# Kernel tuning notes

Measured on AMD Instinct MI355X. Metric: run time of the kernel, lower is better.

## Reference

```python
import jax, jax.numpy as jnp
import numpy as np

N = 100_000      # nodes
E = 800_000      # edges (avg degree 8)
IN = 64          # in_channels
OUT = 64         # out_channels
HEADS = 4
HD = OUT // HEADS  # per-head out channels (concat=True)


def _unif(key, shape, fan_in):
    b = 1.0 / np.sqrt(fan_in)
    return jax.random.uniform(key, shape, jnp.float32, -b, b)


def setup_inputs() -> dict:
    key = jax.random.key(0)
    ks = jax.random.split(key, 12)
    x = jax.random.normal(ks[0], (N, IN), jnp.float32)
    pos = jax.random.normal(ks[1], (N, 3), jnp.float32)
    edge_index = jax.random.randint(ks[2], (2, E), 0, N, jnp.int32)
    # Per-head PointTransformerConv params (stacked over heads).
    # lin / lin_src / lin_dst are bias-free Linear(in, hd); pos_nn is Linear(3, hd) with bias.
    W_lin = _unif(ks[3], (HEADS, IN, HD), IN)
    W_src = _unif(ks[4], (HEADS, IN, HD), IN)
    W_dst = _unif(ks[5], (HEADS, IN, HD), IN)
    W_pos = _unif(ks[6], (HEADS, 3, HD), 3)
    b_pos = _unif(ks[7], (HEADS, HD), 3)
    # projection MLP: Linear(OUT,OUT) -> ReLU -> Linear(OUT,OUT)
    W1 = _unif(ks[8], (OUT, OUT), OUT)
    b1 = _unif(ks[9], (OUT,), OUT)
    W2 = _unif(ks[10], (OUT, OUT), OUT)
    b2 = _unif(ks[11], (OUT,), OUT)
    return dict(x=x, pos=pos, edge_index=edge_index, W_lin=W_lin, W_src=W_src,
                W_dst=W_dst, W_pos=W_pos, b_pos=b_pos, W1=W1, b1=b1, W2=W2, b2=b2)


def reference(x, pos, edge_index, W_lin, W_src, W_dst, W_pos, b_pos, W1, b1, W2, b2):
    # Add self-loops (PointTransformerConv default add_self_loops=True).
    loops = jnp.arange(N, dtype=edge_index.dtype)
    src = jnp.concatenate([edge_index[0], loops])   # j (source)
    dst = jnp.concatenate([edge_index[1], loops])   # i (target)

    # Per-node, all-heads projections: [N, H, HD]
    v = jnp.einsum('ni,hio->nho', x, W_lin)
    a_src = jnp.einsum('ni,hio->nho', x, W_src)
    a_dst = jnp.einsum('ni,hio->nho', x, W_dst)

    # Relative-position encoding delta = pos_nn(pos_i - pos_j): [Et, H, HD]
    rel = pos[dst] - pos[src]
    delta = jnp.einsum('ec,hco->eho', rel, W_pos) + b_pos

    # Attention logits per edge/channel: alpha_i - alpha_j + delta
    alpha = a_dst[dst] - a_src[src] + delta

    # Segment softmax over incoming edges of each target node (numerically stable).
    amax = jax.ops.segment_max(alpha, dst, num_segments=N)
    amax = jnp.where(jnp.isfinite(amax), amax, 0.0)
    ex = jnp.exp(alpha - amax[dst])
    denom = jax.ops.segment_sum(ex, dst, num_segments=N)
    attn = ex / jnp.maximum(denom[dst], 1e-16)

    # Message = attn * (lin(x_j) + delta), scatter-sum to targets: [N, H, HD]
    msg = attn * (v[src] + delta)
    out_h = jax.ops.segment_sum(msg, dst, num_segments=N)

    # Concat heads -> projection MLP
    out = out_h.reshape(N, HEADS * HD)
    h = jax.nn.relu(out @ W1 + b1)
    return h @ W2 + b2
```

## Files before the change

### kernel.cpp

```cpp
#include <hip/hip_runtime.h>
#include <math.h>


typedef _Float16 f16;
typedef _Float16 f16x2 __attribute__((ext_vector_type(2)));
typedef _Float16 f16x4 __attribute__((ext_vector_type(4)));
typedef _Float16 f16x8 __attribute__((ext_vector_type(8)));
typedef float f32x4 __attribute__((ext_vector_type(4)));

#define A_PITCH 104
#define LOG2E 1.44269504f
#define S_CAP 32

__global__ __launch_bounds__(256) void prep_hist_scatter_kernel(
    const int* __restrict__ ei, int E, int Hb,
    int* __restrict__ cnt, int* __restrict__ ssrc,
    const float* __restrict__ Ws, const float* __restrict__ Wl,
    const float* __restrict__ Wp, const float* __restrict__ bp,
    const float* __restrict__ W1, const float* __restrict__ W2,
    f16* __restrict__ Bt, f16* __restrict__ W1p, f16* __restrict__ W2p)
{
    if ((int)blockIdx.x < Hb) {
        int e = blockIdx.x * 256 + threadIdx.x;
        if (e < E) {
            int s = ei[e], d = ei[E + e];
            int r = atomicAdd(&cnt[d], 1);
            if (r < S_CAP) ssrc[d * S_CAP + r] = s;
        }
        return;
    }
    int idx = (blockIdx.x - Hb) * 256 + threadIdx.x;
    if (idx < 192 * 96) {
        int col = idx / 96, k = idx - col * 96;
        float v = 0.f;
        if (col < 128) {
            int p = col >> 1, h = p >> 4, o = p & 15;
            if (col & 1) {
                if (k < 64)      v = Wl[h * 1024 + k * 16 + o];
                else if (k < 67) v = -Wp[h * 48 + (k - 64) * 16 + o];
            } else {
                if (k < 64)      v = -LOG2E * Ws[h * 1024 + k * 16 + o];
                else if (k < 67) v = -LOG2E * Wp[h * 48 + (k - 64) * 16 + o];
            }
        } else {
            int c = col - 128, h = c >> 4, o = c & 15;
            if (k >= 64 && k < 67) v = Wp[h * 48 + (k - 64) * 16 + o];
            else if (k == 67)      v = bp[c];
        }
        Bt[col * 96 + k] = (f16)v;
    } else if (idx < 192 * 96 + 4096) {
        int t = idx - 192 * 96;
        int col = t >> 6, k = t & 63;
        W1p[col * 64 + k] = (f16)W1[k * 64 + col];
    } else if (idx < 192 * 96 + 8192) {
        int t = idx - 192 * 96 - 4096;
        int col = t >> 6, k = t & 63;
        W2p[col * 64 + k] = (f16)W2[k * 64 + col];
    }
}

__global__ __launch_bounds__(256) void gemm_kernel(
    const float* __restrict__ x, const float* __restrict__ pos,
    const f16* __restrict__ Bt, f16* __restrict__ P, int N)
{
    __shared__ f16 As[64 * A_PITCH];
    int tid = threadIdx.x;
    int l = tid & 63, wv = tid >> 6;
    int quad = l >> 4, lr = l & 15;
    int nb = blockIdx.x * 64;

    for (int it = 0; it < 4; it++) {
        int q = it * 256 + tid;
        int n = q >> 4, k = (q & 15) * 4;
        float4 xv = make_float4(0.f, 0.f, 0.f, 0.f);
        if (nb + n < N) xv = *(const float4*)&x[(size_t)(nb + n) * 64 + k];
        f16x4 h4; h4[0] = (f16)xv.x; h4[1] = (f16)xv.y; h4[2] = (f16)xv.z; h4[3] = (f16)xv.w;
        *(f16x4*)&As[n * A_PITCH + k] = h4;
    }
    {
        int n = tid >> 2, seg = tid & 3;
        f16x4 z = {(f16)0, (f16)0, (f16)0, (f16)0};
        f16x4 h4 = z;
        if (seg == 0 && nb + n < N) {
            h4[0] = (f16)pos[(size_t)(nb + n) * 3 + 0];
            h4[1] = (f16)pos[(size_t)(nb + n) * 3 + 1];
            h4[2] = (f16)pos[(size_t)(nb + n) * 3 + 2];
            h4[3] = (f16)1.0f;
        }
        *(f16x4*)&As[n * A_PITCH + 64 + seg * 8] = h4;
        *(f16x4*)&As[n * A_PITCH + 64 + seg * 8 + 4] = z;
    }
    __syncthreads();

    f16x8 af[4][3];
    #pragma unroll
    for (int mt = 0; mt < 4; mt++)
        #pragma unroll
        for (int kt = 0; kt < 3; kt++)
            af[mt][kt] = *(const f16x8*)&As[(mt * 16 + lr) * A_PITCH + kt * 32 + quad * 8];

    #pragma unroll
    for (int t = 0; t < 3; t++) {
        int colBase = (wv * 3 + t) * 16;
        f16x8 b0 = *(const f16x8*)&Bt[(colBase + lr) * 96 + 0  + quad * 8];
        f16x8 b1 = *(const f16x8*)&Bt[(colBase + lr) * 96 + 32 + quad * 8];
        f16x8 b2 = *(const f16x8*)&Bt[(colBase + lr) * 96 + 64 + quad * 8];
        #pragma unroll
        for (int mt = 0; mt < 4; mt++) {
            f32x4 acc = {0.f, 0.f, 0.f, 0.f};
            acc = __builtin_amdgcn_mfma_f32_16x16x32_f16(af[mt][0], b0, acc, 0, 0, 0);
            acc = __builtin_amdgcn_mfma_f32_16x16x32_f16(af[mt][1], b1, acc, 0, 0, 0);
            acc = __builtin_amdgcn_mfma_f32_16x16x32_f16(af[mt][2], b2, acc, 0, 0, 0);
            int col = colBase + lr;
            #pragma unroll
            for (int r = 0; r < 4; r++) {
                int row = nb + mt * 16 + quad * 4 + r;
                if (row < N) P[(size_t)row * 192 + col] = (f16)acc[r];
            }
        }
    }
}

__global__ __launch_bounds__(256) void attn_mlp_kernel(
    const f16* __restrict__ P,
    const int* __restrict__ cnt, const int* __restrict__ ssrc,
    const f16* __restrict__ W1p, const f16* __restrict__ W2p,
    const float* __restrict__ b1, const float* __restrict__ b2,
    float* __restrict__ out, int N)
{
    __shared__ f16 As[64 * 72];
    __shared__ f16 Hs[64 * 72];
    int tid = threadIdx.x, c = tid & 63, wv = tid >> 6;
    int quad = c >> 4, lr = c & 15;
    int nb = blockIdx.x * 64;

    const f16x2* AV = (const f16x2*)P;

    for (int t = 0; t < 16; t++) {
        int i = nb + wv * 16 + t;
        float oh = 0.f;
        if (i < N) {
            float Gi = (float)P[(size_t)i * 192 + 128 + c];
            f16x2 wi = AV[(size_t)i * 96 + c];
            float e0 = __builtin_amdgcn_exp2f((float)wi[0]);
            float num = e0 * (float)wi[1];
            float den = e0;
            int deg = cnt[i]; if (deg > S_CAP) deg = S_CAP;
            int base = i * S_CAP, k = 0;

#define EDGE_STEP(w)                                              \
            {                                                     \
                float e = __builtin_amdgcn_exp2f((float)w[0]);    \
                num = fmaf(e, (float)w[1], num);                  \
                den += e;                                         \
            }
            for (; k + 4 <= deg; k += 4) {
                int j0 = __builtin_amdgcn_readfirstlane(ssrc[base + k]);
                int j1 = __builtin_amdgcn_readfirstlane(ssrc[base + k + 1]);
                int j2 = __builtin_amdgcn_readfirstlane(ssrc[base + k + 2]);
                int j3 = __builtin_amdgcn_readfirstlane(ssrc[base + k + 3]);
                f16x2 w0 = AV[(size_t)j0 * 96 + c];
                f16x2 w1 = AV[(size_t)j1 * 96 + c];
                f16x2 w2 = AV[(size_t)j2 * 96 + c];
                f16x2 w3 = AV[(size_t)j3 * 96 + c];
                EDGE_STEP(w0); EDGE_STEP(w1); EDGE_STEP(w2); EDGE_STEP(w3);
            }
            for (; k < deg; k++) {
                int j = __builtin_amdgcn_readfirstlane(ssrc[base + k]);
                f16x2 w = AV[(size_t)j * 96 + c];
                EDGE_STEP(w);
            }
#undef EDGE_STEP
            oh = num / den + Gi;
        }
        As[(wv * 16 + t) * 72 + c] = (f16)oh;
    }
    __syncthreads();

    f16x8 af[4][2];
    #pragma unroll
    for (int mt = 0; mt < 4; mt++)
        #pragma unroll
        for (int kt = 0; kt < 2; kt++)
            af[mt][kt] = *(const f16x8*)&As[(mt * 16 + lr) * 72 + kt * 32 + quad * 8];

    int col = wv * 16 + lr;
    f16x8 wb0 = *(const f16x8*)&W1p[col * 64 + quad * 8];
    f16x8 wb1 = *(const f16x8*)&W1p[col * 64 + 32 + quad * 8];
    float bias1 = b1[col];
    #pragma unroll
    for (int mt = 0; mt < 4; mt++) {
        f32x4 acc = {0.f, 0.f, 0.f, 0.f};
        acc = __builtin_amdgcn_mfma_f32_16x16x32_f16(af[mt][0], wb0, acc, 0, 0, 0);
        acc = __builtin_amdgcn_mfma_f32_16x16x32_f16(af[mt][1], wb1, acc, 0, 0, 0);
        #pragma unroll
        for (int r = 0; r < 4; r++) {
            int row = mt * 16 + quad * 4 + r;
            Hs[row * 72 + col] = (f16)fmaxf(acc[r] + bias1, 0.f);
        }
    }
    __syncthreads();

    f16x8 ag[4][2];
    #pragma unroll
    for (int mt = 0; mt < 4; mt++)
        #pragma unroll
        for (int kt = 0; kt < 2; kt++)
            ag[mt][kt] = *(const f16x8*)&Hs[(mt * 16 + lr) * 72 + kt * 32 + quad * 8];

    f16x8 wc0 = *(const f16x8*)&W2p[col * 64 + quad * 8];
    f16x8 wc1 = *(const f16x8*)&W2p[col * 64 + 32 + quad * 8];
    float bias2 = b2[col];
    #pragma unroll
    for (int mt = 0; mt < 4; mt++) {
        f32x4 acc = {0.f, 0.f, 0.f, 0.f};
        acc = __builtin_amdgcn_mfma_f32_16x16x32_f16(ag[mt][0], wc0, acc, 0, 0, 0);
        acc = __builtin_amdgcn_mfma_f32_16x16x32_f16(ag[mt][1], wc1, acc, 0, 0, 0);
        #pragma unroll
        for (int r = 0; r < 4; r++) {
            int row = nb + mt * 16 + quad * 4 + r;
            if (row < N) out[(size_t)row * 64 + col] = acc[r] + bias2;
        }
    }
}

extern "C" void kernel_launch(void* const* d_in, const int* in_sizes, int n_in,
                              void* d_out, int out_size, void* d_ws, size_t ws_size,
                              hipStream_t stream)
{
    const float* x    = (const float*)d_in[0];
    const float* pos  = (const float*)d_in[1];
    const int*   ei   = (const int*)d_in[2];
    const float* Wl   = (const float*)d_in[3];
    const float* Ws   = (const float*)d_in[4];
    const float* Wp   = (const float*)d_in[6];
    const float* bpos = (const float*)d_in[7];
    const float* W1   = (const float*)d_in[8];
    const float* b1   = (const float*)d_in[9];
    const float* W2   = (const float*)d_in[10];
    const float* b2   = (const float*)d_in[11];
    float* out = (float*)d_out;

    const int N = in_sizes[0] / 64;
    const int E = in_sizes[2] / 2;

    char* w = (char*)d_ws;
    f16*  P    = (f16*)w;                   w += (size_t)N * 192 * 2;
    f16*  Bt   = (f16*)w;                   w += 192 * 96 * 2;
    f16*  W1p  = (f16*)w;                   w += 4096 * 2;
    f16*  W2p  = (f16*)w;                   w += 4096 * 2;
    int*  cnt  = (int*)w;                   w += (size_t)N * 4;
    int*  ssrc = (int*)w;

    const int Hb = (E + 255) / 256;
    const int Pb = (192 * 96 + 8192 + 255) / 256;

    hipMemsetAsync(cnt, 0, (size_t)N * sizeof(int), stream);

    prep_hist_scatter_kernel<<<Hb + Pb, 256, 0, stream>>>(
        ei, E, Hb, cnt, ssrc, Ws, Wl, Wp, bpos, W1, W2, Bt, W1p, W2p);
    gemm_kernel<<<(N + 63) / 64, 256, 0, stream>>>(x, pos, Bt, P, N);
    attn_mlp_kernel<<<(N + 63) / 64, 256, 0, stream>>>(P, cnt, ssrc, W1p, W2p,
                                                       b1, b2, out, N);
}
```

Measured before the change: 218.5 us.

## Split projection buffer into compact AV and G arrays, coalesce stores, shrink attention tiles

The GEMM output moves from one 192-wide buffer into a 128-wide AV array (gathered per edge) and a separate 64-wide G array. Results are staged through shared memory so global stores are coalesced 16-byte writes, and the edge gather now reads from a denser array. The attention kernel processes 32 nodes per block instead of 64, giving more blocks. Its edge loop becomes a single masked 4-wide loop, which is why the ssrc slots are now zeroed by an enlarged memset, adding extra memset traffic.

```diff
diff --git a/kernel.cpp b/kernel.cpp
--- a/kernel.cpp
+++ b/kernel.cpp
@@ -9,6 +9,7 @@
 typedef float f32x4 __attribute__((ext_vector_type(4)));
 
 #define A_PITCH 104
+#define C_PITCH 200
 #define LOG2E 1.44269504f
 #define S_CAP 32
 
@@ -61,9 +62,10 @@
 
 __global__ __launch_bounds__(256) void gemm_kernel(
     const float* __restrict__ x, const float* __restrict__ pos,
-    const f16* __restrict__ Bt, f16* __restrict__ P, int N)
-{
-    __shared__ f16 As[64 * A_PITCH];
+    const f16* __restrict__ Bt,
+    f16* __restrict__ AV, f16* __restrict__ G, int N)
+{
+    __shared__ f16 smem[64 * C_PITCH];
     int tid = threadIdx.x;
     int l = tid & 63, wv = tid >> 6;
     int quad = l >> 4, lr = l & 15;
@@ -75,7 +77,7 @@
         float4 xv = make_float4(0.f, 0.f, 0.f, 0.f);
         if (nb + n < N) xv = *(const float4*)&x[(size_t)(nb + n) * 64 + k];
         f16x4 h4; h4[0] = (f16)xv.x; h4[1] = (f16)xv.y; h4[2] = (f16)xv.z; h4[3] = (f16)xv.w;
-        *(f16x4*)&As[n * A_PITCH + k] = h4;
+        *(f16x4*)&smem[n * A_PITCH + k] = h4;
     }
     {
         int n = tid >> 2, seg = tid & 3;
@@ -87,8 +89,8 @@
             h4[2] = (f16)pos[(size_t)(nb + n) * 3 + 2];
             h4[3] = (f16)1.0f;
         }
-        *(f16x4*)&As[n * A_PITCH + 64 + seg * 8] = h4;
-        *(f16x4*)&As[n * A_PITCH + 64 + seg * 8 + 4] = z;
+        *(f16x4*)&smem[n * A_PITCH + 64 + seg * 8] = h4;
+        *(f16x4*)&smem[n * A_PITCH + 64 + seg * 8 + 4] = z;
     }
     __syncthreads();
 
@@ -97,7 +99,8 @@
     for (int mt = 0; mt < 4; mt++)
         #pragma unroll
         for (int kt = 0; kt < 3; kt++)
-            af[mt][kt] = *(const f16x8*)&As[(mt * 16 + lr) * A_PITCH + kt * 32 + quad * 8];
+            af[mt][kt] = *(const f16x8*)&smem[(mt * 16 + lr) * A_PITCH + kt * 32 + quad * 8];
+    __syncthreads();
 
     #pragma unroll
     for (int t = 0; t < 3; t++) {
@@ -114,72 +117,87 @@
             int col = colBase + lr;
             #pragma unroll
             for (int r = 0; r < 4; r++) {
-                int row = nb + mt * 16 + quad * 4 + r;
-                if (row < N) P[(size_t)row * 192 + col] = (f16)acc[r];
+                int row = mt * 16 + quad * 4 + r;
+                smem[row * C_PITCH + col] = (f16)acc[r];
             }
         }
     }
+    __syncthreads();
+
+    for (int it = 0; it < 4; it++) {
+        int cid = it * 256 + tid;
+        int row = cid >> 4, off = (cid & 15) * 8;
+        if (nb + row < N)
+            *(f16x8*)&AV[(size_t)(nb + row) * 128 + off] =
+                *(const f16x8*)&smem[row * C_PITCH + off];
+    }
+    for (int it = 0; it < 2; it++) {
+        int cid = it * 256 + tid;
+        int row = cid >> 3, off = (cid & 7) * 8;
+        if (nb + row < N)
+            *(f16x8*)&G[(size_t)(nb + row) * 64 + off] =
+                *(const f16x8*)&smem[row * C_PITCH + 128 + off];
+    }
 }
 
 __global__ __launch_bounds__(256) void attn_mlp_kernel(
-    const f16* __restrict__ P,
+    const f16* __restrict__ AV, const f16* __restrict__ G,
     const int* __restrict__ cnt, const int* __restrict__ ssrc,
     const f16* __restrict__ W1p, const f16* __restrict__ W2p,
     const float* __restrict__ b1, const float* __restrict__ b2,
     float* __restrict__ out, int N)
 {
-    __shared__ f16 As[64 * 72];
-    __shared__ f16 Hs[64 * 72];
+    __shared__ f16 As[32 * 72];
+    __shared__ f16 Hs[32 * 72];
     int tid = threadIdx.x, c = tid & 63, wv = tid >> 6;
     int quad = c >> 4, lr = c & 15;
-    int nb = blockIdx.x * 64;
-
-    const f16x2* AV = (const f16x2*)P;
-
-    for (int t = 0; t < 16; t++) {
-        int i = nb + wv * 16 + t;
+    int nb = blockIdx.x * 32;
+
+    const f16x2* AV2 = (const f16x2*)AV;
+
+    for (int t = 0; t < 8; t++) {
+        int i = __builtin_amdgcn_readfirstlane(nb + wv * 8 + t);
         float oh = 0.f;
         if (i < N) {
-            float Gi = (float)P[(size_t)i * 192 + 128 + c];
-            f16x2 wi = AV[(size_t)i * 96 + c];
+            float Gi = (float)G[(size_t)i * 64 + c];
+            f16x2 wi = AV2[(size_t)i * 64 + c];
             float e0 = __builtin_amdgcn_exp2f((float)wi[0]);
             float num = e0 * (float)wi[1];
             float den = e0;
-            int deg = cnt[i]; if (deg > S_CAP) deg = S_CAP;
-            int base = i * S_CAP, k = 0;
-
-#define EDGE_STEP(w)                                              \
-            {                                                     \
-                float e = __builtin_amdgcn_exp2f((float)w[0]);    \
-                num = fmaf(e, (float)w[1], num);                  \
-                den += e;                                         \
-            }
-            for (; k + 4 <= deg; k += 4) {
+            int deg = __builtin_amdgcn_readfirstlane(cnt[i]);
+            if (deg > S_CAP) deg = S_CAP;
+            int base = i * S_CAP;
+            for (int k = 0; k < deg; k += 4) {
                 int j0 = __builtin_amdgcn_readfirstlane(ssrc[base + k]);
                 int j1 = __builtin_amdgcn_readfirstlane(ssrc[base + k + 1]);
                 int j2 = __builtin_amdgcn_readfirstlane(ssrc[base + k + 2]);
                 int j3 = __builtin_amdgcn_readfirstlane(ssrc[base + k + 3]);
-                f16x2 w0 = AV[(size_t)j0 * 96 + c];
-                f16x2 w1 = AV[(size_t)j1 * 96 + c];
-                f16x2 w2 = AV[(size_t)j2 * 96 + c];
-                f16x2 w3 = AV[(size_t)j3 * 96 + c];
-                EDGE_STEP(w0); EDGE_STEP(w1); EDGE_STEP(w2); EDGE_STEP(w3);
+                f16x2 w0 = AV2[(size_t)j0 * 64 + c];
+                f16x2 w1 = AV2[(size_t)j1 * 64 + c];
+                f16x2 w2 = AV2[(size_t)j2 * 64 + c];
+                f16x2 w3 = AV2[(size_t)j3 * 64 + c];
+                float e;
+                e = __builtin_amdgcn_exp2f((float)w0[0]);
+                num = fmaf(e, (float)w0[1], num); den += e;
+                e = __builtin_amdgcn_exp2f((float)w1[0]);
+                e = (k + 1 < deg) ? e : 0.f;
+                num = fmaf(e, (float)w1[1], num); den += e;
+                e = __builtin_amdgcn_exp2f((float)w2[0]);
+                e = (k + 2 < deg) ? e : 0.f;
+                num = fmaf(e, (float)w2[1], num); den += e;
+                e = __builtin_amdgcn_exp2f((float)w3[0]);
+                e = (k + 3 < deg) ? e : 0.f;
+                num = fmaf(e, (float)w3[1], num); den += e;
             }
-            for (; k < deg; k++) {
-                int j = __builtin_amdgcn_readfirstlane(ssrc[base + k]);
-                f16x2 w = AV[(size_t)j * 96 + c];
-                EDGE_STEP(w);
-            }
-#undef EDGE_STEP
             oh = num / den + Gi;
         }
-        As[(wv * 16 + t) * 72 + c] = (f16)oh;
-    }
-    __syncthreads();
-
-    f16x8 af[4][2];
-    #pragma unroll
-    for (int mt = 0; mt < 4; mt++)
+        As[(wv * 8 + t) * 72 + c] = (f16)oh;
+    }
+    __syncthreads();
+
+    f16x8 af[2][2];
+    #pragma unroll
+    for (int mt = 0; mt < 2; mt++)
         #pragma unroll
         for (int kt = 0; kt < 2; kt++)
             af[mt][kt] = *(const f16x8*)&As[(mt * 16 + lr) * 72 + kt * 32 + quad * 8];
@@ -189,7 +207,7 @@
     f16x8 wb1 = *(const f16x8*)&W1p[col * 64 + 32 + quad * 8];
     float bias1 = b1[col];
     #pragma unroll
-    for (int mt = 0; mt < 4; mt++) {
+    for (int mt = 0; mt < 2; mt++) {
         f32x4 acc = {0.f, 0.f, 0.f, 0.f};
         acc = __builtin_amdgcn_mfma_f32_16x16x32_f16(af[mt][0], wb0, acc, 0, 0, 0);
         acc = __builtin_amdgcn_mfma_f32_16x16x32_f16(af[mt][1], wb1, acc, 0, 0, 0);
@@ -201,9 +219,9 @@
     }
     __syncthreads();
 
-    f16x8 ag[4][2];
-    #pragma unroll
-    for (int mt = 0; mt < 4; mt++)
+    f16x8 ag[2][2];
+    #pragma unroll
+    for (int mt = 0; mt < 2; mt++)
         #pragma unroll
         for (int kt = 0; kt < 2; kt++)
             ag[mt][kt] = *(const f16x8*)&Hs[(mt * 16 + lr) * 72 + kt * 32 + quad * 8];
@@ -212,7 +230,7 @@
     f16x8 wc1 = *(const f16x8*)&W2p[col * 64 + 32 + quad * 8];
     float bias2 = b2[col];
     #pragma unroll
-    for (int mt = 0; mt < 4; mt++) {
+    for (int mt = 0; mt < 2; mt++) {
         f32x4 acc = {0.f, 0.f, 0.f, 0.f};
         acc = __builtin_amdgcn_mfma_f32_16x16x32_f16(ag[mt][0], wc0, acc, 0, 0, 0);
         acc = __builtin_amdgcn_mfma_f32_16x16x32_f16(ag[mt][1], wc1, acc, 0, 0, 0);
@@ -245,21 +263,22 @@
     const int E = in_sizes[2] / 2;
 
     char* w = (char*)d_ws;
-    f16*  P    = (f16*)w;                   w += (size_t)N * 192 * 2;
+    f16*  AV   = (f16*)w;                   w += (size_t)N * 128 * 2;
+    f16*  G    = (f16*)w;                   w += (size_t)N * 64 * 2;
     f16*  Bt   = (f16*)w;                   w += 192 * 96 * 2;
     f16*  W1p  = (f16*)w;                   w += 4096 * 2;
     f16*  W2p  = (f16*)w;                   w += 4096 * 2;
     int*  cnt  = (int*)w;                   w += (size_t)N * 4;
-    int*  ssrc = (int*)w;
+    int*  ssrc = (int*)w;                   w += (size_t)N * S_CAP * 4;
 
     const int Hb = (E + 255) / 256;
     const int Pb = (192 * 96 + 8192 + 255) / 256;
 
-    hipMemsetAsync(cnt, 0, (size_t)N * sizeof(int), stream);
+    hipMemsetAsync(cnt, 0, (size_t)N * (1 + S_CAP) * sizeof(int), stream);
 
     prep_hist_scatter_kernel<<<Hb + Pb, 256, 0, stream>>>(
         ei, E, Hb, cnt, ssrc, Ws, Wl, Wp, bpos, W1, W2, Bt, W1p, W2p);
-    gemm_kernel<<<(N + 63) / 64, 256, 0, stream>>>(x, pos, Bt, P, N);
-    attn_mlp_kernel<<<(N + 63) / 64, 256, 0, stream>>>(P, cnt, ssrc, W1p, W2p,
+    gemm_kernel<<<(N + 63) / 64, 256, 0, stream>>>(x, pos, Bt, AV, G, N);
+    attn_mlp_kernel<<<(N + 31) / 32, 256, 0, stream>>>(AV, G, cnt, ssrc, W1p, W2p,
                                                        b1, b2, out, N);
 }
```

Result: faster. 205.4 us (-6.0%).
